# Performance work log

Measured on AMD Instinct MI355X. Metric: run time of the kernel, lower is better.

Reference implementation:

```python
import jax, jax.numpy as jnp
import numpy as np

N_NODES = 50000
N_EDGES = 800000
D = 64          # encoder output dim (encoder.out)
MLP_DIM = 64    # mlp_edge_model hidden dim


def setup_inputs() -> dict:
    key = jax.random.key(0)
    ks = jax.random.split(key, 8)
    x = jax.random.normal(ks[0], (N_NODES, D), dtype=jnp.float32)
    edge_index = jax.random.randint(ks[1], (2, N_EDGES), 0, N_NODES, dtype=jnp.int64)
    # xavier-ish scaled weights
    W_enc = jax.random.normal(ks[2], (D, D), dtype=jnp.float32) * (1.0 / np.sqrt(D))
    b_enc = jnp.zeros((D,), dtype=jnp.float32)
    W1 = jax.random.normal(ks[3], (2 * D, MLP_DIM), dtype=jnp.float32) * (1.0 / np.sqrt(2 * D))
    b1 = jnp.zeros((MLP_DIM,), dtype=jnp.float32)
    W2 = jax.random.normal(ks[4], (MLP_DIM, 1), dtype=jnp.float32) * (1.0 / np.sqrt(MLP_DIM))
    b2 = jnp.zeros((1,), dtype=jnp.float32)
    return {"x": x, "edge_index": edge_index, "W_enc": W_enc, "b_enc": b_enc,
            "W1": W1, "b1": b1, "W2": W2, "b2": b2}


def reference(x, edge_index, W_enc, b_enc, W1, b1, W2, b2):
    src, dst = edge_index[0], edge_index[1]
    # --- encoder: 1-layer message-passing GCN stand-in ---
    agg = jax.ops.segment_sum(x[src], dst, num_segments=N_NODES)   # [N, D]
    node_emb = jax.nn.relu((x + agg) @ W_enc + b_enc)              # [N, D]
    # --- gather src/dst embeddings, concat, 2-layer MLP edge scorer ---
    edge_emb = jnp.concatenate([node_emb[src], node_emb[dst]], axis=1)  # [E, 2D]
    h = jax.nn.relu(edge_emb @ W1 + b1)                            # [E, mlp_dim]
    edge_logits = h @ W2 + b2                                      # [E, 1]
    return edge_logits
```

## Files before the change

### kernel.cpp

```cpp
#include <hip/hip_runtime.h>
#include <hip/hip_bf16.h>
#include <stdint.h>

#define N_NODES 50000
#define N_EDGES 800000
#define D 64
#define VROWS 50048
#define CVT_BLOCKS 3125
#define CAP 64

typedef __hip_bfloat16 bf16;
typedef __bf16 bf16x8 __attribute__((ext_vector_type(8)));
typedef float  f32x4  __attribute__((ext_vector_type(4)));

__device__ __forceinline__ float bu2f(unsigned short u) {
    unsigned int w = ((unsigned int)u) << 16;
    return __builtin_bit_cast(float, w);
}
__device__ __forceinline__ unsigned short f2bu(float f) {
    bf16 h = __float2bfloat16(f);
    return __builtin_bit_cast(unsigned short, h);
}
__device__ __forceinline__ float ldf(const void* p, size_t i, bool f32mode) {
    if (f32mode) return ((const float*)p)[i];
    return bu2f(((const unsigned short*)p)[i]);
}
__device__ __forceinline__ void stf(void* p, size_t i, float v, bool f32mode) {
    if (f32mode) ((float*)p)[i] = v;
    else ((unsigned short*)p)[i] = f2bu(v);
}
__device__ __forceinline__ int ldidx(const int* ei, size_t e, int row, bool i64mode) {
    if (i64mode) return ei[((size_t)row * N_EDGES + e) * 2];
    return ei[(size_t)row * N_EDGES + e];
}
__device__ __forceinline__ void unpack8(uint4 v, float* f) {
    f[0] = bu2f(v.x & 0xffff); f[1] = bu2f(v.x >> 16);
    f[2] = bu2f(v.y & 0xffff); f[3] = bu2f(v.y >> 16);
    f[4] = bu2f(v.z & 0xffff); f[5] = bu2f(v.z >> 16);
    f[6] = bu2f(v.w & 0xffff); f[7] = bu2f(v.w >> 16);
}

__global__ __launch_bounds__(256) void init_kernel(
    const void* __restrict__ x, const int* __restrict__ ei,
    const void* __restrict__ W2, const void* __restrict__ b1,
    const void* __restrict__ b2,
    int* __restrict__ flags, unsigned short* __restrict__ w2bf,
    float* __restrict__ b1f, float* __restrict__ b2fp,
    int* __restrict__ counts,
    unsigned short* __restrict__ xbf,
    unsigned short* __restrict__ dst16, unsigned short* __restrict__ src16)
{
    __shared__ int sh_f32m, sh_i64m;
    int tid = threadIdx.x;

    if (tid < 64) {
        const unsigned short* u = (const unsigned short*)x;
        int weird = 0, zeros = 0;
        #pragma unroll
        for (int k = tid; k < 128; k += 64) {
            int ex = (u[2 * k] >> 7) & 0xFF;
            if (ex < 90 || ex > 160) ++weird;
            if (ei[2 * k + 1] == 0) ++zeros;
        }
        #pragma unroll
        for (int off = 1; off < 64; off <<= 1) {
            weird += __shfl_xor(weird, off, 64);
            zeros += __shfl_xor(zeros, off, 64);
        }
        if (tid == 0) {
            sh_f32m = (weird > 32) ? 1 : 0;
            sh_i64m = (zeros > 120) ? 1 : 0;
        }
    }
    __syncthreads();
    bool f32m = sh_f32m != 0;
    bool i64m = sh_i64m != 0;

    if (blockIdx.x == 0) {
        if (tid < 64) {
            w2bf[tid] = f2bu(ldf(W2, tid, f32m));
            b1f[tid]  = ldf(b1, tid, f32m);
        }
        if (tid == 0) {
            flags[0] = f32m ? 1 : 0;
            flags[1] = sh_i64m;
            b2fp[0] = ldf(b2, 0, f32m);
        }
    }

    int cbase = blockIdx.x * 16 + (tid & 15);
    if (tid < 16 && cbase < N_NODES) counts[cbase] = 0;

    int e = blockIdx.x * 256 + tid;
    dst16[e] = (unsigned short)ldidx(ei, e, 1, i64m);
    src16[e] = (unsigned short)ldidx(ei, e, 0, i64m);

    size_t idx4 = (size_t)blockIdx.x * 256 + tid;
    if (f32m) {
        float4 fv = ((const float4*)x)[idx4];
        ushort4 o;
        o.x = f2bu(fv.x); o.y = f2bu(fv.y); o.z = f2bu(fv.z); o.w = f2bu(fv.w);
        ((ushort4*)xbf)[idx4] = o;
    } else {
        ((uint2*)xbf)[idx4] = ((const uint2*)x)[idx4];
    }
}

__global__ __launch_bounds__(256) void histfill_kernel(
    const unsigned short* __restrict__ dst16,
    const unsigned short* __restrict__ src16,
    int* __restrict__ counts, unsigned short* __restrict__ sarr)
{
    int region = blockIdx.x >> 3;
    int grp    = blockIdx.x & 7;
    int e0 = region * 2048 + threadIdx.x * 8;
    if (e0 >= N_EDGES) return;
    uint4 dv = *(const uint4*)(dst16 + e0);
    uint4 sv = *(const uint4*)(src16 + e0);
    unsigned int dw[4] = {dv.x, dv.y, dv.z, dv.w};
    unsigned int sw[4] = {sv.x, sv.y, sv.z, sv.w};
    #pragma unroll
    for (int k = 0; k < 8; ++k) {
        if (e0 + k >= N_EDGES) break;
        int d = (int)((dw[k >> 1] >> ((k & 1) * 16)) & 0xffffu);
        if (((d >> 6) & 7) != grp) continue;
        int r = atomicAdd(&counts[d], 1);
        if (r < CAP)
            sarr[(size_t)d * CAP + r] =
                (unsigned short)((sw[k >> 1] >> ((k & 1) * 16)) & 0xffffu);
    }
}

__global__ __launch_bounds__(256) void gather_kernel(
    const unsigned short* __restrict__ xbf,
    const int* __restrict__ counts, const unsigned short* __restrict__ sarr,
    unsigned short* __restrict__ vtab)
{
    int w    = (blockIdx.x * 256 + threadIdx.x) >> 6;
    int lane = threadIdx.x & 63;
    if (w >= N_NODES) return;
    int cnt = counts[w];
    if (cnt > CAP) cnt = CAP;
    int beg = w * CAP, end = beg + cnt;
    int f8   = lane & 7;
    int slot = lane >> 3;

    float acc[8] = {0.f, 0.f, 0.f, 0.f, 0.f, 0.f, 0.f, 0.f};
    if (slot == 0) {
        uint4 q = ((const uint4*)xbf)[(size_t)w * 8 + f8];
        unpack8(q, acc);
    }

    int j = beg;
    for (; j + 16 <= end; j += 16) {
        int s0 = sarr[j + slot];
        int s1 = sarr[j + 8 + slot];
        uint4 q0 = ((const uint4*)xbf)[(size_t)s0 * 8 + f8];
        uint4 q1 = ((const uint4*)xbf)[(size_t)s1 * 8 + f8];
        float f0[8], f1[8];
        unpack8(q0, f0);
        unpack8(q1, f1);
        #pragma unroll
        for (int i = 0; i < 8; ++i) acc[i] += f0[i] + f1[i];
    }
    for (; j < end; j += 8) {
        int e = j + slot;
        bool ok = e < end;
        int s = sarr[ok ? e : beg];
        uint4 q = ((const uint4*)xbf)[(size_t)s * 8 + f8];
        float f[8];
        unpack8(q, f);
        if (ok) {
            #pragma unroll
            for (int i = 0; i < 8; ++i) acc[i] += f[i];
        }
    }

    #pragma unroll
    for (int i = 0; i < 8; ++i) {
        acc[i] += __shfl_xor(acc[i], 8, 64);
        acc[i] += __shfl_xor(acc[i], 16, 64);
        acc[i] += __shfl_xor(acc[i], 32, 64);
    }

    if (slot == 0) {
        uint4 o;
        o.x = (unsigned int)f2bu(acc[0]) | ((unsigned int)f2bu(acc[1]) << 16);
        o.y = (unsigned int)f2bu(acc[2]) | ((unsigned int)f2bu(acc[3]) << 16);
        o.z = (unsigned int)f2bu(acc[4]) | ((unsigned int)f2bu(acc[5]) << 16);
        o.w = (unsigned int)f2bu(acc[6]) | ((unsigned int)f2bu(acc[7]) << 16);
        ((uint4*)vtab)[(size_t)w * 8 + f8] = o;
    }
}

__global__ __launch_bounds__(256) void nodemm_kernel(
    const unsigned short* vtab,
    const void* __restrict__ W_enc, const void* __restrict__ b_enc,
    const void* __restrict__ W1,
    unsigned short* p_src, unsigned short* p_dst,
    const float* __restrict__ b1f, const int* __restrict__ flags)
{
    __shared__ unsigned short wtWe[64 * 72];
    __shared__ unsigned short wtWa[64 * 72];
    __shared__ unsigned short wtWb[64 * 72];
    __shared__ float benc[64];
    __shared__ unsigned short ebuf[4][16 * 72];

    bool f32m = flags[0] != 0;
    int tid = threadIdx.x;
    for (int t = tid; t < 4096; t += 256) {
        int i = t >> 6, j = t & 63;
        wtWe[j * 72 + i] = f2bu(ldf(W_enc, t, f32m));
        wtWa[j * 72 + i] = f2bu(ldf(W1, t, f32m));
        wtWb[j * 72 + i] = f2bu(ldf(W1, 4096 + t, f32m));
    }
    if (tid < 64) benc[tid] = ldf(b_enc, tid, f32m);
    __syncthreads();

    int wave = tid >> 6;
    int lane = tid & 63;
    int lo   = lane & 15;
    int quad = lane >> 4;
    unsigned short* eb = ebuf[wave];
    int base = blockIdx.x * 64 + wave * 16;

    bf16x8 av0 = *(const bf16x8*)&vtab[(size_t)(base + lo) * D + quad * 8];
    bf16x8 av1 = *(const bf16x8*)&vtab[(size_t)(base + lo) * D + 32 + quad * 8];

    f32x4 z = {0.f, 0.f, 0.f, 0.f};
    f32x4 acc1[4] = {z, z, z, z};
    #pragma unroll
    for (int nt = 0; nt < 4; ++nt) {
        bf16x8 b0  = *(const bf16x8*)&wtWe[(nt * 16 + lo) * 72 + quad * 8];
        bf16x8 b1v = *(const bf16x8*)&wtWe[(nt * 16 + lo) * 72 + 32 + quad * 8];
        acc1[nt] = __builtin_amdgcn_mfma_f32_16x16x32_bf16(av0, b0, acc1[nt], 0, 0, 0);
        acc1[nt] = __builtin_amdgcn_mfma_f32_16x16x32_bf16(av1, b1v, acc1[nt], 0, 0, 0);
    }
    #pragma unroll
    for (int nt = 0; nt < 4; ++nt) {
        float bias = benc[nt * 16 + lo];
        #pragma unroll
        for (int r = 0; r < 4; ++r) {
            int m = quad * 4 + r;
            float ev = fmaxf(acc1[nt][r] + bias, 0.f);
            eb[m * 72 + nt * 16 + lo] = f2bu(ev);
        }
    }

    bf16x8 ae0 = *(const bf16x8*)&eb[lo * 72 + quad * 8];
    bf16x8 ae1 = *(const bf16x8*)&eb[lo * 72 + 32 + quad * 8];

    f32x4 acc2[4] = {z, z, z, z};
    f32x4 acc3[4] = {z, z, z, z};
    #pragma unroll
    for (int nt = 0; nt < 4; ++nt) {
        bf16x8 ba0 = *(const bf16x8*)&wtWa[(nt * 16 + lo) * 72 + quad * 8];
        bf16x8 ba1 = *(const bf16x8*)&wtWa[(nt * 16 + lo) * 72 + 32 + quad * 8];
        bf16x8 bb0 = *(const bf16x8*)&wtWb[(nt * 16 + lo) * 72 + quad * 8];
        bf16x8 bb1 = *(const bf16x8*)&wtWb[(nt * 16 + lo) * 72 + 32 + quad * 8];
        acc2[nt] = __builtin_amdgcn_mfma_f32_16x16x32_bf16(ae0, ba0, acc2[nt], 0, 0, 0);
        acc2[nt] = __builtin_amdgcn_mfma_f32_16x16x32_bf16(ae1, ba1, acc2[nt], 0, 0, 0);
        acc3[nt] = __builtin_amdgcn_mfma_f32_16x16x32_bf16(ae0, bb0, acc3[nt], 0, 0, 0);
        acc3[nt] = __builtin_amdgcn_mfma_f32_16x16x32_bf16(ae1, bb1, acc3[nt], 0, 0, 0);
    }
    #pragma unroll
    for (int nt = 0; nt < 4; ++nt) {
        float b1v = b1f[nt * 16 + lo];
        #pragma unroll
        for (int r = 0; r < 4; ++r) {
            int node = base + quad * 4 + r;
            if (node < N_NODES) {
                size_t idx = (size_t)node * D + nt * 16 + lo;
                p_src[idx] = f2bu(acc2[nt][r] + b1v);
                p_dst[idx] = f2bu(acc3[nt][r]);
            }
        }
    }
}

__global__ __launch_bounds__(256) void edge_kernel(
    const unsigned short* __restrict__ p_src,
    const unsigned short* __restrict__ p_dst,
    const unsigned short* __restrict__ src16,
    const unsigned short* __restrict__ dst16,
    const unsigned short* __restrict__ w2bf, const float* __restrict__ b2fp,
    void* __restrict__ out, const int* __restrict__ flags)
{
    bool f32m = flags[0] != 0;
    int wid  = (blockIdx.x * 256 + threadIdx.x) >> 6;
    int lane = threadIdx.x & 63;
    int e_base = wid * 16;
    if (e_base >= N_EDGES) return;
    int g   = lane >> 3;
    int sub = lane & 7;

    uint4 w2v = ((const uint4*)w2bf)[sub];
    float w2[8];
    unpack8(w2v, w2);
    float bb = b2fp[0];

    int e0 = e_base + g;
    int e1 = e_base + 8 + g;
    int s0 = src16[e0], d0 = dst16[e0];
    int s1 = src16[e1], d1 = dst16[e1];

    uint4 qs0 = ((const uint4*)p_src)[(size_t)s0 * 8 + sub];
    uint4 qd0 = ((const uint4*)p_dst)[(size_t)d0 * 8 + sub];
    uint4 qs1 = ((const uint4*)p_src)[(size_t)s1 * 8 + sub];
    uint4 qd1 = ((const uint4*)p_dst)[(size_t)d1 * 8 + sub];
    float fs0[8], fd0[8], fs1[8], fd1[8];
    unpack8(qs0, fs0);
    unpack8(qd0, fd0);
    unpack8(qs1, fs1);
    unpack8(qd1, fd1);

    float c0 = 0.f, c1 = 0.f;
    #pragma unroll
    for (int i = 0; i < 8; ++i) {
        c0 += fmaxf(fs0[i] + fd0[i], 0.f) * w2[i];
        c1 += fmaxf(fs1[i] + fd1[i], 0.f) * w2[i];
    }
    c0 += __shfl_xor(c0, 1, 64);
    c0 += __shfl_xor(c0, 2, 64);
    c0 += __shfl_xor(c0, 4, 64);
    c1 += __shfl_xor(c1, 1, 64);
    c1 += __shfl_xor(c1, 2, 64);
    c1 += __shfl_xor(c1, 4, 64);
    if (sub == 0) {
        stf(out, e0, c0 + bb, f32m);
        stf(out, e1, c1 + bb, f32m);
    }
}

extern "C" void kernel_launch(void* const* d_in, const int* in_sizes, int n_in,
                              void* d_out, int out_size, void* d_ws, size_t ws_size,
                              hipStream_t stream)
{
    const void* x     = d_in[0];
    const int*  ei    = (const int*)d_in[1];
    const void* W_enc = d_in[2];
    const void* b_enc = d_in[3];
    const void* W1    = d_in[4];
    const void* b1    = d_in[5];
    const void* W2    = d_in[6];
    const void* b2    = d_in[7];

    const size_t NTv  = (size_t)VROWS * D;
    const size_t NCAP = (size_t)N_NODES * CAP;
    unsigned short* p_src = (unsigned short*)d_ws;
    unsigned short* p_dst = p_src + NTv;
    unsigned short* xbf   = p_dst + NTv;
    unsigned short* sarr  = xbf + NTv;
    float* b1f     = (float*)(sarr + NCAP);
    unsigned short* w2bf = (unsigned short*)(b1f + 64);
    float* b2fp    = (float*)(w2bf + 64);
    int*   counts  = (int*)(b2fp + 4);
    int*   flags   = counts + N_NODES;
    unsigned short* dst16 = (unsigned short*)(flags + 8);
    unsigned short* src16 = dst16 + N_EDGES;

    unsigned short* vtab = p_src;

    init_kernel<<<CVT_BLOCKS, 256, 0, stream>>>(x, ei, W2, b1, b2, flags, w2bf,
                                                b1f, b2fp, counts, xbf,
                                                dst16, src16);

    const int HF_BLOCKS = ((N_EDGES + 2047) / 2048) * 8;
    histfill_kernel<<<HF_BLOCKS, 256, 0, stream>>>(dst16, src16, counts, sarr);

    const int NWB = (N_NODES * 64 + 255) / 256;
    gather_kernel<<<NWB, 256, 0, stream>>>(xbf, counts, sarr, vtab);
    nodemm_kernel<<<(N_NODES + 63) / 64, 256, 0, stream>>>(vtab, W_enc, b_enc, W1,
                                                           p_src, p_dst, b1f, flags);
    edge_kernel<<<NWB, 256, 0, stream>>>(p_src, p_dst, src16, dst16,
                                         w2bf, b2fp, d_out, flags);
}
```

Before: 182.3 us.

## Fuse index conversion and x bf16 conversion into histogram fill kernel

Splits the old init kernel into a tiny flag/zeroing kernel and folds the x-to-bf16 conversion and edge-index narrowing into the histogram-fill kernel, which now reads the raw edge_index directly. This removes one pass that writes dst16/src16 and then re-reads them, at the cost of each of the 8 group blocks re-reading the raw (possibly int64, strided) indices per region. That is eight times more raw index traffic, served mostly from cache. Every block also reads the flags from global memory.

```diff
diff --git a/kernel.cpp b/kernel.cpp
--- a/kernel.cpp
+++ b/kernel.cpp
@@ -40,20 +40,16 @@
     f[6] = bu2f(v.w & 0xffff); f[7] = bu2f(v.w >> 16);
 }
 
-__global__ __launch_bounds__(256) void init_kernel(
+__global__ __launch_bounds__(256) void initA_kernel(
     const void* __restrict__ x, const int* __restrict__ ei,
     const void* __restrict__ W2, const void* __restrict__ b1,
     const void* __restrict__ b2,
     int* __restrict__ flags, unsigned short* __restrict__ w2bf,
     float* __restrict__ b1f, float* __restrict__ b2fp,
-    int* __restrict__ counts,
-    unsigned short* __restrict__ xbf,
-    unsigned short* __restrict__ dst16, unsigned short* __restrict__ src16)
-{
-    __shared__ int sh_f32m, sh_i64m;
+    int* __restrict__ counts)
+{
     int tid = threadIdx.x;
-
-    if (tid < 64) {
+    if (blockIdx.x == 0 && tid < 64) {
         const unsigned short* u = (const unsigned short*)x;
         int weird = 0, zeros = 0;
         #pragma unroll
@@ -67,67 +63,60 @@
             weird += __shfl_xor(weird, off, 64);
             zeros += __shfl_xor(zeros, off, 64);
         }
-        if (tid == 0) {
-            sh_f32m = (weird > 32) ? 1 : 0;
-            sh_i64m = (zeros > 120) ? 1 : 0;
-        }
-    }
-    __syncthreads();
-    bool f32m = sh_f32m != 0;
-    bool i64m = sh_i64m != 0;
-
-    if (blockIdx.x == 0) {
-        if (tid < 64) {
-            w2bf[tid] = f2bu(ldf(W2, tid, f32m));
-            b1f[tid]  = ldf(b1, tid, f32m);
-        }
+        bool f32m = (weird > 32);
+        w2bf[tid] = f2bu(ldf(W2, tid, f32m));
+        b1f[tid]  = ldf(b1, tid, f32m);
         if (tid == 0) {
             flags[0] = f32m ? 1 : 0;
-            flags[1] = sh_i64m;
+            flags[1] = (zeros > 120) ? 1 : 0;
             b2fp[0] = ldf(b2, 0, f32m);
         }
     }
-
-    int cbase = blockIdx.x * 16 + (tid & 15);
-    if (tid < 16 && cbase < N_NODES) counts[cbase] = 0;
-
-    int e = blockIdx.x * 256 + tid;
-    dst16[e] = (unsigned short)ldidx(ei, e, 1, i64m);
-    src16[e] = (unsigned short)ldidx(ei, e, 0, i64m);
-
-    size_t idx4 = (size_t)blockIdx.x * 256 + tid;
-    if (f32m) {
-        float4 fv = ((const float4*)x)[idx4];
-        ushort4 o;
-        o.x = f2bu(fv.x); o.y = f2bu(fv.y); o.z = f2bu(fv.z); o.w = f2bu(fv.w);
-        ((ushort4*)xbf)[idx4] = o;
-    } else {
-        ((uint2*)xbf)[idx4] = ((const uint2*)x)[idx4];
-    }
-}
-
-__global__ __launch_bounds__(256) void histfill_kernel(
-    const unsigned short* __restrict__ dst16,
-    const unsigned short* __restrict__ src16,
-    int* __restrict__ counts, unsigned short* __restrict__ sarr)
-{
-    int region = blockIdx.x >> 3;
-    int grp    = blockIdx.x & 7;
-    int e0 = region * 2048 + threadIdx.x * 8;
-    if (e0 >= N_EDGES) return;
-    uint4 dv = *(const uint4*)(dst16 + e0);
-    uint4 sv = *(const uint4*)(src16 + e0);
-    unsigned int dw[4] = {dv.x, dv.y, dv.z, dv.w};
-    unsigned int sw[4] = {sv.x, sv.y, sv.z, sv.w};
+    int i = blockIdx.x * 256 + tid;
+    if (i < N_NODES) counts[i] = 0;
+}
+
+__global__ __launch_bounds__(256) void histconv_kernel(
+    const void* __restrict__ x, const int* __restrict__ ei,
+    const int* __restrict__ flags,
+    int* __restrict__ counts, unsigned short* __restrict__ sarr,
+    unsigned short* __restrict__ xbf,
+    unsigned short* __restrict__ dst16, unsigned short* __restrict__ src16)
+{
+    bool f32m = flags[0] != 0;
+    bool i64m = flags[1] != 0;
+    int tid = threadIdx.x;
+    int bid = blockIdx.x;
+
+    if (bid < CVT_BLOCKS) {
+        size_t idx4 = (size_t)bid * 256 + tid;
+        if (f32m) {
+            float4 fv = ((const float4*)x)[idx4];
+            ushort4 o;
+            o.x = f2bu(fv.x); o.y = f2bu(fv.y); o.z = f2bu(fv.z); o.w = f2bu(fv.w);
+            ((ushort4*)xbf)[idx4] = o;
+        } else {
+            ((uint2*)xbf)[idx4] = ((const uint2*)x)[idx4];
+        }
+    }
+
+    int region = bid >> 3;
+    int grp    = bid & 7;
+    int e0 = region * 2048 + tid * 8;
     #pragma unroll
     for (int k = 0; k < 8; ++k) {
-        if (e0 + k >= N_EDGES) break;
-        int d = (int)((dw[k >> 1] >> ((k & 1) * 16)) & 0xffffu);
+        int e = e0 + k;
+        if (e >= N_EDGES) break;
+        int d = ldidx(ei, e, 1, i64m);
+        int s = ldidx(ei, e, 0, i64m);
+        if (grp == 0) {
+            dst16[e] = (unsigned short)d;
+            src16[e] = (unsigned short)s;
+        }
         if (((d >> 6) & 7) != grp) continue;
         int r = atomicAdd(&counts[d], 1);
         if (r < CAP)
-            sarr[(size_t)d * CAP + r] =
-                (unsigned short)((sw[k >> 1] >> ((k & 1) * 16)) & 0xffffu);
+            sarr[(size_t)d * CAP + r] = (unsigned short)s;
     }
 }
 
@@ -361,12 +350,13 @@
 
     unsigned short* vtab = p_src;
 
-    init_kernel<<<CVT_BLOCKS, 256, 0, stream>>>(x, ei, W2, b1, b2, flags, w2bf,
-                                                b1f, b2fp, counts, xbf,
-                                                dst16, src16);
+    const int NBLKA = (N_NODES + 255) / 256;
+    initA_kernel<<<NBLKA, 256, 0, stream>>>(x, ei, W2, b1, b2,
+                                            flags, w2bf, b1f, b2fp, counts);
 
     const int HF_BLOCKS = ((N_EDGES + 2047) / 2048) * 8;
-    histfill_kernel<<<HF_BLOCKS, 256, 0, stream>>>(dst16, src16, counts, sarr);
+    histconv_kernel<<<HF_BLOCKS, 256, 0, stream>>>(x, ei, flags, counts, sarr,
+                                                   xbf, dst16, src16);
 
     const int NWB = (N_NODES * 64 + 255) / 256;
     gather_kernel<<<NWB, 256, 0, stream>>>(xbf, counts, sarr, vtab);
```

Measured after the change: 225.5 us. 23.7% more time.
